# Kernel tuning notes

Hardware: AMD Instinct MI355X
Metric: run time of the kernel (lower is better)

Reference implementation:

```python
import jax, jax.numpy as jnp
import numpy as np

B, S, D, H = 4, 1024, 1024, 16
DK = D // H


def setup_inputs() -> dict:
    key = jax.random.key(0)
    ks = jax.random.split(key, 14)
    scale = 1.0 / np.sqrt(D)
    inp = {
        "Qx": jax.random.normal(ks[0], (B, S, D), jnp.float32),
        "Kx": jax.random.normal(ks[1], (B, S, D), jnp.float32),
        "Vx": jax.random.normal(ks[2], (B, S, D), jnp.float32),
        "prob_phn": jax.random.uniform(ks[3], (B, S, S), jnp.float32),
        "mask": jax.random.randint(ks[4], (B, S, S), 0, 2, jnp.int32),
        "lambda_val": 1,
        "Wq": jax.random.normal(ks[5], (D, D), jnp.float32) * scale,
        "bq": jnp.zeros((D,), jnp.float32),
        "Wk": jax.random.normal(ks[6], (D, D), jnp.float32) * scale,
        "bk": jnp.zeros((D,), jnp.float32),
        "Wv": jax.random.normal(ks[7], (D, D), jnp.float32) * scale,
        "bv": jnp.zeros((D,), jnp.float32),
        "Wo": jax.random.normal(ks[8], (D, D), jnp.float32) * scale,
        "bo": jnp.zeros((D,), jnp.float32),
    }
    return inp


def _split_heads(x):
    # [B,S,D] -> [B,H,S,DK]
    b, s, _ = x.shape
    return x.reshape(b, s, H, DK).transpose(0, 2, 1, 3)


def reference(Qx, Kx, Vx, prob_phn, mask, lambda_val, Wq, bq, Wk, bk, Wv, bv, Wo, bo):
    q = _split_heads(Qx @ Wq.T + bq)
    k = _split_heads(Kx @ Wk.T + bk)
    v = _split_heads(Vx @ Wv.T + bv)
    scores = jnp.einsum("bhqd,bhkd->bhqk", q, k) / jnp.sqrt(jnp.float32(DK))
    if lambda_val > 0:
        # prob_phn: [B,S,S] -> transpose last two dims, broadcast over heads
        scores = scores - lambda_val * jnp.swapaxes(prob_phn, -2, -1)[:, None]
    scores = jnp.where(mask[:, None] == 0, jnp.float32(-1e9), scores)
    probs = jax.nn.softmax(scores, axis=-1)
    attn = jnp.einsum("bhqk,bhkd->bhqd", probs, v)
    out = attn.transpose(0, 2, 1, 3).reshape(Qx.shape[0], Qx.shape[1], D)
    out = out @ Wo.T + bo
    return (out, mask)
```

## Files before the change

kernel.cpp:

```cpp
#include <hip/hip_runtime.h>
#include <hip/hip_bf16.h>
#include <cstdint>
#include <cstddef>

#define BB 4
#define SS 1024
#define DD 1024
#define HH 16
#define DKK 64

typedef unsigned short u16;
typedef __bf16 bf16_t;
typedef __attribute__((ext_vector_type(8))) bf16_t bf16x8;
typedef __attribute__((ext_vector_type(4))) float floatx4;

static __device__ inline u16 f2bf(float f) {
    union { float f; unsigned u; } v; v.f = f;
    unsigned r = v.u + 0x7fffu + ((v.u >> 16) & 1u);
    return (u16)(r >> 16);
}

static __device__ inline void load16_lds(const void* g, void* l) {
    __builtin_amdgcn_global_load_lds(
        (const __attribute__((address_space(1))) unsigned int*)g,
        (__attribute__((address_space(3))) unsigned int*)l,
        16, 0, 0);
}

static __device__ inline int swz64(int row, int c) { return row * 64 + ((c ^ (row & 7)) * 8); }
static __device__ inline int swz32(int row, int c) { return row * 32 + ((c ^ ((row >> 1) & 3)) * 8); }

__global__ void cvt_all_kernel(const float* __restrict__ Qx, const float* __restrict__ Kx,
                               const float* __restrict__ Vx,
                               const float* __restrict__ Wq, const float* __restrict__ Wk,
                               const float* __restrict__ Wv, const float* __restrict__ Wo,
                               u16* __restrict__ Xq, u16* __restrict__ Xk, u16* __restrict__ Xv,
                               u16* __restrict__ wq, u16* __restrict__ wk,
                               u16* __restrict__ wv, u16* __restrict__ wo)
{
    int u = blockIdx.x * blockDim.x + threadIdx.x;
    const float* src; u16* dst; int off;
    if (u < 3145728) {
        int s = u >> 20;  off = u & 1048575;
        src = (s == 0) ? Qx : (s == 1) ? Kx : Vx;
        dst = (s == 0) ? Xq : (s == 1) ? Xk : Xv;
    } else {
        int v2 = u - 3145728;
        int s = v2 >> 18;  off = v2 & 262143;
        src = (s == 0) ? Wq : (s == 1) ? Wk : (s == 2) ? Wv : Wo;
        dst = (s == 0) ? wq : (s == 1) ? wk : (s == 2) ? wv : wo;
    }
    float4 f = ((const float4*)src)[off];
    ushort4 r;
    r.x = f2bf(f.x); r.y = f2bf(f.y); r.z = f2bf(f.z); r.w = f2bf(f.w);
    ((ushort4*)dst)[off] = r;
}

static __device__ inline float lam_val(const int* p) {
    int v = *p;
    if (v >= -100000 && v <= 100000) return (float)v;
    union { int i; float f; } u; u.i = v; return u.f;
}

__global__ void bias_kernel(const float* __restrict__ prob, const int* __restrict__ mask,
                            const int* __restrict__ lam_p, float* __restrict__ biasT,
                            float* __restrict__ maskOut)
{
    __shared__ float tile[32][33];
    const int b = blockIdx.z;
    const int q0 = blockIdx.x * 32, k0 = blockIdx.y * 32;
    const int tx = threadIdx.x, ty = threadIdx.y;
    tile[ty][tx] = prob[((size_t)b * SS + (k0 + ty)) * SS + (q0 + tx)];
    __syncthreads();
    const float lam = lam_val(lam_p);
    const size_t oidx = ((size_t)b * SS + (q0 + ty)) * SS + (k0 + tx);
    int mi = mask[oidx];
    biasT[oidx] = (mi == 0) ? -1e9f : -lam * tile[tx][ty];
    if (maskOut) maskOut[oidx] = (float)mi;
}

template <bool F32OUT>
static __device__ inline void gemm_body(const u16* __restrict__ A, const u16* __restrict__ W,
                                        const float* __restrict__ bias,
                                        u16* __restrict__ Cb, float* __restrict__ Cf)
{
    constexpr int K = 1024, N = 1024;
    __shared__ __align__(16) u16 As[128 * 32];
    __shared__ __align__(16) u16 Bs[128 * 32];
    const int tid = threadIdx.x;
    const int wv = tid >> 6, ln = tid & 63, l15 = ln & 15, quad = ln >> 4;
    const int mBase = blockIdx.y * 128;
    const int nBase = blockIdx.x * 128;
    const int wm = (wv & 1) * 64, wn = (wv >> 1) * 64;

    const u16* Aptr[2]; const u16* Wptr[2];
    #pragma unroll
    for (int r = 0; r < 2; ++r) {
        int p = r * 256 + wv * 64 + ln;
        int row = p >> 2;
        int c = (p & 3) ^ ((row >> 1) & 3);
        Aptr[r] = A + (size_t)(mBase + row) * K + c * 8;
        Wptr[r] = W + (size_t)(nBase + row) * K + c * 8;
    }

    floatx4 acc[4][4] = {};

    for (int k0 = 0; k0 < K; k0 += 32) {
        __syncthreads();
        #pragma unroll
        for (int r = 0; r < 2; ++r) {
            load16_lds(Aptr[r] + k0, &As[(r * 256 + wv * 64) * 8]);
            load16_lds(Wptr[r] + k0, &Bs[(r * 256 + wv * 64) * 8]);
        }
        __syncthreads();
        bf16x8 af[4], bfr[4];
        #pragma unroll
        for (int i = 0; i < 4; ++i)
            af[i] = *(const bf16x8*)&As[swz32(wm + i * 16 + l15, quad)];
        #pragma unroll
        for (int j = 0; j < 4; ++j)
            bfr[j] = *(const bf16x8*)&Bs[swz32(wn + j * 16 + l15, quad)];
        #pragma unroll
        for (int i = 0; i < 4; ++i)
            #pragma unroll
            for (int j = 0; j < 4; ++j)
                acc[i][j] = __builtin_amdgcn_mfma_f32_16x16x32_bf16(af[i], bfr[j], acc[i][j], 0, 0, 0);
    }

    #pragma unroll
    for (int i = 0; i < 4; ++i) {
        #pragma unroll
        for (int j = 0; j < 4; ++j) {
            int col = nBase + wn + j * 16 + l15;
            float bcol = bias[col];
            #pragma unroll
            for (int r = 0; r < 4; ++r) {
                int row = mBase + wm + i * 16 + quad * 4 + r;
                float v = acc[i][j][r] + bcol;
                if (F32OUT) Cf[(size_t)row * N + col] = v;
                else        Cb[(size_t)row * N + col] = f2bf(v);
            }
        }
    }
}

__global__ __launch_bounds__(256) void gemm_qkv_kernel(
    const u16* __restrict__ Xq, const u16* __restrict__ Xk, const u16* __restrict__ Xv,
    const u16* __restrict__ Wq, const u16* __restrict__ Wk, const u16* __restrict__ Wv,
    const float* __restrict__ bq, const float* __restrict__ bk, const float* __restrict__ bv,
    u16* __restrict__ Cq, u16* __restrict__ Ck, u16* __restrict__ Cv)
{
    const int z = blockIdx.z;
    const u16* A = (z == 0) ? Xq : (z == 1) ? Xk : Xv;
    const u16* W = (z == 0) ? Wq : (z == 1) ? Wk : Wv;
    const float* bias = (z == 0) ? bq : (z == 1) ? bk : bv;
    u16* C = (z == 0) ? Cq : (z == 1) ? Ck : Cv;
    gemm_body<false>(A, W, bias, C, nullptr);
}

__global__ __launch_bounds__(256) void gemm_out_kernel(
    const u16* __restrict__ A, const u16* __restrict__ W,
    const float* __restrict__ bias, float* __restrict__ Cf)
{
    gemm_body<true>(A, W, bias, nullptr, Cf);
}

__global__ void vtrans_kernel(const u16* __restrict__ vf, u16* __restrict__ vt)
{
    __shared__ u16 tile[64][66];
    const int st = blockIdx.x, h = blockIdx.y, b = blockIdx.z;
    const int tx = threadIdx.x;
    const int ty = threadIdx.y;
    #pragma unroll
    for (int r = 0; r < 4; ++r) {
        int s = st * 64 + r * 16 + ty;
        tile[r * 16 + ty][tx] = vf[((size_t)(b * SS + s)) * DD + h * DKK + tx];
    }
    __syncthreads();
    #pragma unroll
    for (int r = 0; r < 4; ++r) {
        int dk = r * 16 + ty;
        vt[((size_t)((b * HH + h) * DKK) + dk) * SS + st * 64 + tx] = tile[tx][dk];
    }
}

__global__ __launch_bounds__(256) void attn_kernel(
    const u16* __restrict__ Qf, const u16* __restrict__ Kf,
    const u16* __restrict__ Vt, const float* __restrict__ biasT,
    u16* __restrict__ Attn)
{
    __shared__ __align__(16) u16 Qs[64 * 64];
    __shared__ __align__(16) u16 Ks[64 * 64];
    __shared__ __align__(16) u16 Vs[64 * 64];
    __shared__ __align__(16) u16 Ps[4][16 * 72];
    const int tid = threadIdx.x;
    const int wv = tid >> 6, ln = tid & 63, l15 = ln & 15, quad = ln >> 4;
    const int qt = blockIdx.x, h = blockIdx.y, b = blockIdx.z;
    const int q0 = qt * 64;

    int row_s[2], col_s[2];
    #pragma unroll
    for (int r = 0; r < 2; ++r) {
        int p = r * 256 + wv * 64 + ln;
        int row = p >> 3;
        int c = (p & 7) ^ (row & 7);
        row_s[r] = row; col_s[r] = c * 8;
    }

    #pragma unroll
    for (int r = 0; r < 2; ++r)
        load16_lds(Qf + ((size_t)(b * SS + q0 + row_s[r])) * DD + h * DKK + col_s[r],
                   &Qs[(r * 256 + wv * 64) * 8]);
    __syncthreads();

    bf16x8 aq[2];
    #pragma unroll
    for (int t = 0; t < 2; ++t)
        aq[t] = *(const bf16x8*)&Qs[swz64(wv * 16 + l15, t * 4 + quad)];

    const size_t vt_head = ((size_t)(b * HH + h)) * DKK * SS;
    const u16* Kptr[2]; const u16* Vptr[2];
    #pragma unroll
    for (int r = 0; r < 2; ++r) {
        Kptr[r] = Kf + ((size_t)(b * SS + row_s[r])) * DD + h * DKK + col_s[r];
        Vptr[r] = Vt + vt_head + (size_t)row_s[r] * SS + col_s[r];
    }
    const float* biasRow = biasT + ((size_t)b * SS + q0 + wv * 16 + quad * 4) * SS + l15;

    floatx4 o[4] = {};
    float rsum[4] = {0.f, 0.f, 0.f, 0.f};

    float bv_[4][4];
    #pragma unroll
    for (int j = 0; j < 4; ++j)
        #pragma unroll
        for (int r = 0; r < 4; ++r)
            bv_[j][r] = biasRow[(size_t)r * SS + j * 16];

    for (int kt = 0; kt < 16; ++kt) {
        const int kk0 = kt * 64;
        __syncthreads();
        #pragma unroll
        for (int r = 0; r < 2; ++r) {
            load16_lds(Kptr[r] + (size_t)kk0 * DD, &Ks[(r * 256 + wv * 64) * 8]);
            load16_lds(Vptr[r] + kk0, &Vs[(r * 256 + wv * 64) * 8]);
        }
        __syncthreads();

        floatx4 sfr[4];
        #pragma unroll
        for (int j = 0; j < 4; ++j) {
            bf16x8 bk0 = *(const bf16x8*)&Ks[swz64(j * 16 + l15, quad)];
            bf16x8 bk1 = *(const bf16x8*)&Ks[swz64(j * 16 + l15, 4 + quad)];
            floatx4 s = {};
            s = __builtin_amdgcn_mfma_f32_16x16x32_bf16(aq[0], bk0, s, 0, 0, 0);
            s = __builtin_amdgcn_mfma_f32_16x16x32_bf16(aq[1], bk1, s, 0, 0, 0);
            sfr[j] = s;
        }

        #pragma unroll
        for (int j = 0; j < 4; ++j)
            #pragma unroll
            for (int r = 0; r < 4; ++r) {
                float p = __expf(fmaf(sfr[j][r], 0.125f, bv_[j][r]));
                unsigned pu = __float_as_uint(p);
                rsum[r] += __uint_as_float(pu & 0xffff0000u);
                Ps[wv][(quad * 4 + r) * 72 + j * 16 + l15] = (u16)(pu >> 16);
            }

        if (kt < 15) {
            #pragma unroll
            for (int j = 0; j < 4; ++j)
                #pragma unroll
                for (int r = 0; r < 4; ++r)
                    bv_[j][r] = biasRow[(size_t)r * SS + kk0 + 64 + j * 16];
        }

        #pragma unroll
        for (int t = 0; t < 2; ++t) {
            bf16x8 ap = *(const bf16x8*)&Ps[wv][l15 * 72 + t * 32 + quad * 8];
            #pragma unroll
            for (int j = 0; j < 4; ++j) {
                bf16x8 bvv = *(const bf16x8*)&Vs[swz64(j * 16 + l15, t * 4 + quad)];
                o[j] = __builtin_amdgcn_mfma_f32_16x16x32_bf16(ap, bvv, o[j], 0, 0, 0);
            }
        }
    }

    #pragma unroll
    for (int r = 0; r < 4; ++r) {
        float s = rsum[r];
        s += __shfl_xor(s, 1);
        s += __shfl_xor(s, 2);
        s += __shfl_xor(s, 4);
        s += __shfl_xor(s, 8);
        rsum[r] = 1.0f / s;
    }
    #pragma unroll
    for (int j = 0; j < 4; ++j) {
        #pragma unroll
        for (int r = 0; r < 4; ++r) {
            int srow = q0 + wv * 16 + quad * 4 + r;
            int dk = j * 16 + l15;
            Attn[((size_t)(b * SS + srow)) * DD + h * DKK + dk] = f2bf(o[j][r] * rsum[r]);
        }
    }
}

extern "C" void kernel_launch(void* const* d_in, const int* in_sizes, int n_in,
                              void* d_out, int out_size, void* d_ws, size_t ws_size,
                              hipStream_t stream)
{
    const float* Qx  = (const float*)d_in[0];
    const float* Kx  = (const float*)d_in[1];
    const float* Vx  = (const float*)d_in[2];
    const float* prob = (const float*)d_in[3];
    const int*   mask = (const int*)d_in[4];
    const int*   lam  = (const int*)d_in[5];
    const float* Wq  = (const float*)d_in[6];
    const float* bq  = (const float*)d_in[7];
    const float* Wk  = (const float*)d_in[8];
    const float* bk  = (const float*)d_in[9];
    const float* Wv  = (const float*)d_in[10];
    const float* bv  = (const float*)d_in[11];
    const float* Wo  = (const float*)d_in[12];
    const float* bo  = (const float*)d_in[13];

    char* ws = (char*)d_ws;
    const size_t MB = 1024 * 1024;
    u16*   Xq     = (u16*)(ws + 0 * MB);
    u16*   Xk     = (u16*)(ws + 8 * MB);
    u16*   Xv     = (u16*)(ws + 16 * MB);
    u16*   wq     = (u16*)(ws + 24 * MB);
    u16*   wk     = (u16*)(ws + 26 * MB);
    u16*   wvp    = (u16*)(ws + 28 * MB);
    u16*   wo     = (u16*)(ws + 30 * MB);
    u16*   q_flat = (u16*)(ws + 32 * MB);
    u16*   k_flat = (u16*)(ws + 40 * MB);
    u16*   v_flat = (u16*)(ws + 48 * MB);
    u16*   vt     = (u16*)(ws + 56 * MB);
    float* biasT  = (float*)(ws + 64 * MB);
    u16*   attn   = (u16*)(ws + 80 * MB);

    float* maskOut = (out_size >= 2 * BB * SS * DD) ? (float*)d_out + (size_t)BB * SS * DD
                                                    : nullptr;

    cvt_all_kernel<<<16384, 256, 0, stream>>>(Qx, Kx, Vx, Wq, Wk, Wv, Wo,
                                              Xq, Xk, Xv, wq, wk, wvp, wo);
    bias_kernel<<<dim3(32, 32, 4), dim3(32, 32), 0, stream>>>(prob, mask, lam, biasT, maskOut);
    gemm_qkv_kernel<<<dim3(8, 32, 3), 256, 0, stream>>>(Xq, Xk, Xv, wq, wk, wvp,
                                                        bq, bk, bv, q_flat, k_flat, v_flat);
    vtrans_kernel<<<dim3(16, 16, 4), dim3(64, 16), 0, stream>>>(v_flat, vt);
    attn_kernel<<<dim3(16, 16, 4), 256, 0, stream>>>(q_flat, k_flat, vt, biasT, attn);
    gemm_out_kernel<<<dim3(8, 32, 1), 256, 0, stream>>>(attn, wo, bo, (float*)d_out);
}
```

Before: 268.8 us.

## Fuse V transpose into QKV GEMM epilogue and double query rows per attention block

The V projection GEMM now writes its output directly in the per-head transposed [B,H,DK,S] layout using 4-wide stores, so the separate transpose kernel and its extra round trip through global memory are removed. The attention kernel now handles 128 query rows per block (32 per wave, two MFMA row tiles), so each K/V tile loaded into LDS serves twice as many queries. This halves the grid and raises register and LDS use per block. The row sum now accumulates the full fp32 probability instead of its bf16-truncated value.

New measurement: 268.3 us. About the same (-0.2%).

```diff
diff --git a/kernel.cpp b/kernel.cpp
--- a/kernel.cpp
+++ b/kernel.cpp
@@ -79,7 +79,7 @@
     if (maskOut) maskOut[oidx] = (float)mi;
 }
 
-template <bool F32OUT>
+template <int MODE>
 static __device__ inline void gemm_body(const u16* __restrict__ A, const u16* __restrict__ W,
                                         const float* __restrict__ bias,
                                         u16* __restrict__ Cb, float* __restrict__ Cf)
@@ -133,12 +133,24 @@
         for (int j = 0; j < 4; ++j) {
             int col = nBase + wn + j * 16 + l15;
             float bcol = bias[col];
-            #pragma unroll
-            for (int r = 0; r < 4; ++r) {
-                int row = mBase + wm + i * 16 + quad * 4 + r;
-                float v = acc[i][j][r] + bcol;
-                if (F32OUT) Cf[(size_t)row * N + col] = v;
-                else        Cb[(size_t)row * N + col] = f2bf(v);
+            if (MODE == 2) {
+                int hh = col >> 6, dk = col & 63;
+                int row0 = mBase + wm + i * 16 + quad * 4;
+                int bb = row0 >> 10, s = row0 & 1023;
+                ushort4 v4;
+                v4.x = f2bf(acc[i][j][0] + bcol);
+                v4.y = f2bf(acc[i][j][1] + bcol);
+                v4.z = f2bf(acc[i][j][2] + bcol);
+                v4.w = f2bf(acc[i][j][3] + bcol);
+                *(ushort4*)&Cb[((size_t)((bb * HH + hh) * DKK) + dk) * SS + s] = v4;
+            } else {
+                #pragma unroll
+                for (int r = 0; r < 4; ++r) {
+                    int row = mBase + wm + i * 16 + quad * 4 + r;
+                    float v = acc[i][j][r] + bcol;
+                    if (MODE == 1) Cf[(size_t)row * N + col] = v;
+                    else           Cb[(size_t)row * N + col] = f2bf(v);
+                }
             }
         }
     }
@@ -148,40 +160,25 @@
     const u16* __restrict__ Xq, const u16* __restrict__ Xk, const u16* __restrict__ Xv,
     const u16* __restrict__ Wq, const u16* __restrict__ Wk, const u16* __restrict__ Wv,
     const float* __restrict__ bq, const float* __restrict__ bk, const float* __restrict__ bv,
-    u16* __restrict__ Cq, u16* __restrict__ Ck, u16* __restrict__ Cv)
+    u16* __restrict__ Cq, u16* __restrict__ Ck, u16* __restrict__ Vtout)
 {
     const int z = blockIdx.z;
-    const u16* A = (z == 0) ? Xq : (z == 1) ? Xk : Xv;
-    const u16* W = (z == 0) ? Wq : (z == 1) ? Wk : Wv;
-    const float* bias = (z == 0) ? bq : (z == 1) ? bk : bv;
-    u16* C = (z == 0) ? Cq : (z == 1) ? Ck : Cv;
-    gemm_body<false>(A, W, bias, C, nullptr);
+    if (z == 2) {
+        gemm_body<2>(Xv, Wv, bv, Vtout, nullptr);
+    } else {
+        const u16* A = (z == 0) ? Xq : Xk;
+        const u16* W = (z == 0) ? Wq : Wk;
+        const float* bias = (z == 0) ? bq : bk;
+        u16* C = (z == 0) ? Cq : Ck;
+        gemm_body<0>(A, W, bias, C, nullptr);
+    }
 }
 
 __global__ __launch_bounds__(256) void gemm_out_kernel(
     const u16* __restrict__ A, const u16* __restrict__ W,
     const float* __restrict__ bias, float* __restrict__ Cf)
 {
-    gemm_body<true>(A, W, bias, nullptr, Cf);
-}
-
-__global__ void vtrans_kernel(const u16* __restrict__ vf, u16* __restrict__ vt)
-{
-    __shared__ u16 tile[64][66];
-    const int st = blockIdx.x, h = blockIdx.y, b = blockIdx.z;
-    const int tx = threadIdx.x;
-    const int ty = threadIdx.y;
-    #pragma unroll
-    for (int r = 0; r < 4; ++r) {
-        int s = st * 64 + r * 16 + ty;
-        tile[r * 16 + ty][tx] = vf[((size_t)(b * SS + s)) * DD + h * DKK + tx];
-    }
-    __syncthreads();
-    #pragma unroll
-    for (int r = 0; r < 4; ++r) {
-        int dk = r * 16 + ty;
-        vt[((size_t)((b * HH + h) * DKK) + dk) * SS + st * 64 + tx] = tile[tx][dk];
-    }
+    gemm_body<1>(A, W, bias, nullptr, Cf);
 }
 
 __global__ __launch_bounds__(256) void attn_kernel(
@@ -189,122 +186,150 @@
     const u16* __restrict__ Vt, const float* __restrict__ biasT,
     u16* __restrict__ Attn)
 {
-    __shared__ __align__(16) u16 Qs[64 * 64];
+    __shared__ __align__(16) u16 Qs[128 * 64];
     __shared__ __align__(16) u16 Ks[64 * 64];
     __shared__ __align__(16) u16 Vs[64 * 64];
-    __shared__ __align__(16) u16 Ps[4][16 * 72];
+    __shared__ __align__(16) u16 Ps[4][32 * 72];
     const int tid = threadIdx.x;
     const int wv = tid >> 6, ln = tid & 63, l15 = ln & 15, quad = ln >> 4;
     const int qt = blockIdx.x, h = blockIdx.y, b = blockIdx.z;
-    const int q0 = qt * 64;
-
-    int row_s[2], col_s[2];
+    const int q0 = qt * 128;
+
+    int row64[2], col64[2];
     #pragma unroll
     for (int r = 0; r < 2; ++r) {
         int p = r * 256 + wv * 64 + ln;
+        row64[r] = p >> 3;
+        col64[r] = ((p & 7) ^ (row64[r] & 7)) * 8;
+    }
+
+    #pragma unroll
+    for (int r = 0; r < 4; ++r) {
+        int p = r * 256 + wv * 64 + ln;
         int row = p >> 3;
-        int c = (p & 7) ^ (row & 7);
-        row_s[r] = row; col_s[r] = c * 8;
-    }
-
-    #pragma unroll
-    for (int r = 0; r < 2; ++r)
-        load16_lds(Qf + ((size_t)(b * SS + q0 + row_s[r])) * DD + h * DKK + col_s[r],
+        int c = ((p & 7) ^ (row & 7)) * 8;
+        load16_lds(Qf + ((size_t)(b * SS + q0 + row)) * DD + h * DKK + c,
                    &Qs[(r * 256 + wv * 64) * 8]);
+    }
     __syncthreads();
 
-    bf16x8 aq[2];
-    #pragma unroll
-    for (int t = 0; t < 2; ++t)
-        aq[t] = *(const bf16x8*)&Qs[swz64(wv * 16 + l15, t * 4 + quad)];
+    bf16x8 aq[2][2];
+    #pragma unroll
+    for (int m = 0; m < 2; ++m)
+        #pragma unroll
+        for (int t = 0; t < 2; ++t)
+            aq[m][t] = *(const bf16x8*)&Qs[swz64(wv * 32 + m * 16 + l15, t * 4 + quad)];
 
     const size_t vt_head = ((size_t)(b * HH + h)) * DKK * SS;
-    const u16* Kptr[2]; const u16* Vptr[2];
+    const u16* Kp[2]; const u16* Vp[2];
     #pragma unroll
     for (int r = 0; r < 2; ++r) {
-        Kptr[r] = Kf + ((size_t)(b * SS + row_s[r])) * DD + h * DKK + col_s[r];
-        Vptr[r] = Vt + vt_head + (size_t)row_s[r] * SS + col_s[r];
-    }
-    const float* biasRow = biasT + ((size_t)b * SS + q0 + wv * 16 + quad * 4) * SS + l15;
-
-    floatx4 o[4] = {};
-    float rsum[4] = {0.f, 0.f, 0.f, 0.f};
-
-    float bv_[4][4];
-    #pragma unroll
-    for (int j = 0; j < 4; ++j)
+        Kp[r] = Kf + ((size_t)(b * SS + row64[r])) * DD + h * DKK + col64[r];
+        Vp[r] = Vt + vt_head + (size_t)row64[r] * SS + col64[r];
+    }
+
+    const float* bp[2][4];
+    #pragma unroll
+    for (int m = 0; m < 2; ++m)
         #pragma unroll
         for (int r = 0; r < 4; ++r)
-            bv_[j][r] = biasRow[(size_t)r * SS + j * 16];
+            bp[m][r] = biasT + ((size_t)(b * SS + q0 + wv * 32 + m * 16 + quad * 4 + r)) * SS + l15;
+
+    float bv_[2][4][4];
+    #pragma unroll
+    for (int m = 0; m < 2; ++m)
+        #pragma unroll
+        for (int j = 0; j < 4; ++j)
+            #pragma unroll
+            for (int r = 0; r < 4; ++r)
+                bv_[m][j][r] = bp[m][r][j * 16];
+
+    floatx4 o[2][4] = {};
+    float rsum[2][4] = {};
 
     for (int kt = 0; kt < 16; ++kt) {
-        const int kk0 = kt * 64;
         __syncthreads();
         #pragma unroll
         for (int r = 0; r < 2; ++r) {
-            load16_lds(Kptr[r] + (size_t)kk0 * DD, &Ks[(r * 256 + wv * 64) * 8]);
-            load16_lds(Vptr[r] + kk0, &Vs[(r * 256 + wv * 64) * 8]);
+            load16_lds(Kp[r], &Ks[(r * 256 + wv * 64) * 8]);
+            load16_lds(Vp[r], &Vs[(r * 256 + wv * 64) * 8]);
         }
         __syncthreads();
 
-        floatx4 sfr[4];
+        floatx4 sfr[2][4];
         #pragma unroll
         for (int j = 0; j < 4; ++j) {
             bf16x8 bk0 = *(const bf16x8*)&Ks[swz64(j * 16 + l15, quad)];
             bf16x8 bk1 = *(const bf16x8*)&Ks[swz64(j * 16 + l15, 4 + quad)];
-            floatx4 s = {};
-            s = __builtin_amdgcn_mfma_f32_16x16x32_bf16(aq[0], bk0, s, 0, 0, 0);
-            s = __builtin_amdgcn_mfma_f32_16x16x32_bf16(aq[1], bk1, s, 0, 0, 0);
-            sfr[j] = s;
-        }
-
-        #pragma unroll
-        for (int j = 0; j < 4; ++j)
-            #pragma unroll
-            for (int r = 0; r < 4; ++r) {
-                float p = __expf(fmaf(sfr[j][r], 0.125f, bv_[j][r]));
-                unsigned pu = __float_as_uint(p);
-                rsum[r] += __uint_as_float(pu & 0xffff0000u);
-                Ps[wv][(quad * 4 + r) * 72 + j * 16 + l15] = (u16)(pu >> 16);
+            #pragma unroll
+            for (int m = 0; m < 2; ++m) {
+                floatx4 s = {};
+                s = __builtin_amdgcn_mfma_f32_16x16x32_bf16(aq[m][0], bk0, s, 0, 0, 0);
+                sfr[m][j] = __builtin_amdgcn_mfma_f32_16x16x32_bf16(aq[m][1], bk1, s, 0, 0, 0);
             }
-
-        if (kt < 15) {
+        }
+
+        #pragma unroll
+        for (int m = 0; m < 2; ++m)
             #pragma unroll
             for (int j = 0; j < 4; ++j)
                 #pragma unroll
-                for (int r = 0; r < 4; ++r)
-                    bv_[j][r] = biasRow[(size_t)r * SS + kk0 + 64 + j * 16];
+                for (int r = 0; r < 4; ++r) {
+                    float p = __expf(fmaf(sfr[m][j][r], 0.125f, bv_[m][j][r]));
+                    rsum[m][r] += p;
+                    Ps[wv][(m * 16 + quad * 4 + r) * 72 + j * 16 + l15] =
+                        (u16)(__float_as_uint(p) >> 16);
+                }
+
+        #pragma unroll
+        for (int r = 0; r < 2; ++r) { Kp[r] += (size_t)64 * DD; Vp[r] += 64; }
+        if (kt < 15) {
+            #pragma unroll
+            for (int m = 0; m < 2; ++m)
+                #pragma unroll
+                for (int r = 0; r < 4; ++r) {
+                    bp[m][r] += 64;
+                    #pragma unroll
+                    for (int j = 0; j < 4; ++j)
+                        bv_[m][j][r] = bp[m][r][j * 16];
+                }
         }
 
         #pragma unroll
         for (int t = 0; t < 2; ++t) {
-            bf16x8 ap = *(const bf16x8*)&Ps[wv][l15 * 72 + t * 32 + quad * 8];
+            bf16x8 ap0 = *(const bf16x8*)&Ps[wv][l15 * 72 + t * 32 + quad * 8];
+            bf16x8 ap1 = *(const bf16x8*)&Ps[wv][(16 + l15) * 72 + t * 32 + quad * 8];
             #pragma unroll
             for (int j = 0; j < 4; ++j) {
                 bf16x8 bvv = *(const bf16x8*)&Vs[swz64(j * 16 + l15, t * 4 + quad)];
-                o[j] = __builtin_amdgcn_mfma_f32_16x16x32_bf16(ap, bvv, o[j], 0, 0, 0);
+                o[0][j] = __builtin_amdgcn_mfma_f32_16x16x32_bf16(ap0, bvv, o[0][j], 0, 0, 0);
+                o[1][j] = __builtin_amdgcn_mfma_f32_16x16x32_bf16(ap1, bvv, o[1][j], 0, 0, 0);
             }
         }
     }
 
     #pragma unroll
-    for (int r = 0; r < 4; ++r) {
-        float s = rsum[r];
-        s += __shfl_xor(s, 1);
-        s += __shfl_xor(s, 2);
-        s += __shfl_xor(s, 4);
-        s += __shfl_xor(s, 8);
-        rsum[r] = 1.0f / s;
-    }
-    #pragma unroll
-    for (int j = 0; j < 4; ++j) {
+    for (int m = 0; m < 2; ++m)
         #pragma unroll
         for (int r = 0; r < 4; ++r) {
-            int srow = q0 + wv * 16 + quad * 4 + r;
-            int dk = j * 16 + l15;
-            Attn[((size_t)(b * SS + srow)) * DD + h * DKK + dk] = f2bf(o[j][r] * rsum[r]);
-        }
-    }
+            float s = rsum[m][r];
+            s += __shfl_xor(s, 1);
+            s += __shfl_xor(s, 2);
+            s += __shfl_xor(s, 4);
+            s += __shfl_xor(s, 8);
+            rsum[m][r] = 1.0f / s;
+        }
+    #pragma unroll
+    for (int m = 0; m < 2; ++m)
+        #pragma unroll
+        for (int j = 0; j < 4; ++j)
+            #pragma unroll
+            for (int r = 0; r < 4; ++r) {
+                int srow = q0 + wv * 32 + m * 16 + quad * 4 + r;
+                int dk = j * 16 + l15;
+                Attn[((size_t)(b * SS + srow)) * DD + h * DKK + dk] =
+                    f2bf(o[m][j][r] * rsum[m][r]);
+            }
 }
 
 extern "C" void kernel_launch(void* const* d_in, const int* in_sizes, int n_in,
@@ -337,7 +362,6 @@
     u16*   wo     = (u16*)(ws + 30 * MB);
     u16*   q_flat = (u16*)(ws + 32 * MB);
     u16*   k_flat = (u16*)(ws + 40 * MB);
-    u16*   v_flat = (u16*)(ws + 48 * MB);
     u16*   vt     = (u16*)(ws + 56 * MB);
     float* biasT  = (float*)(ws + 64 * MB);
     u16*   attn   = (u16*)(ws + 80 * MB);
@@ -349,8 +373,7 @@
                                               Xq, Xk, Xv, wq, wk, wvp, wo);
     bias_kernel<<<dim3(32, 32, 4), dim3(32, 32), 0, stream>>>(prob, mask, lam, biasT, maskOut);
     gemm_qkv_kernel<<<dim3(8, 32, 3), 256, 0, stream>>>(Xq, Xk, Xv, wq, wk, wvp,
-                                                        bq, bk, bv, q_flat, k_flat, v_flat);
-    vtrans_kernel<<<dim3(16, 16, 4), dim3(64, 16), 0, stream>>>(v_flat, vt);
-    attn_kernel<<<dim3(16, 16, 4), 256, 0, stream>>>(q_flat, k_flat, vt, biasT, attn);
+                                                        bq, bk, bv, q_flat, k_flat, vt);
+    attn_kernel<<<dim3(8, 16, 4), 256, 0, stream>>>(q_flat, k_flat, vt, biasT, attn);
     gemm_out_kernel<<<dim3(8, 32, 1), 256, 0, stream>>>(attn, wo, bo, (float*)d_out);
 }
```
